# Kernel optimization log

Hardware: AMD Instinct MI355X
Metric: run time of the kernel (lower is better)

The kernel has to match this reference:

```python
import jax, jax.numpy as jnp
import numpy as np

# ---- config constants (from configs) ----
B, L, C = 32, 512, 16
DM, DS, DCONV, EXP, EL = 128, 16, 4, 2, 2
PATCH, STRIDE, PAD, PRED = 16, 8, 8, 96
DIN = EXP * DM            # 256
DTR = (DM + 15) // 16     # dt_rank = 8
NPATCH = (L + 2 * PAD - PATCH) // STRIDE + 1   # 65
HNF = DM * NPATCH         # 8320
EPS = 1e-5


def setup_inputs() -> dict:
    key = jax.random.key(0)
    ks = jax.random.split(key, 14)
    n = jax.random.normal
    A_log = jnp.tile(jnp.log(jnp.arange(1, DS + 1, dtype=jnp.float32)), (EL, DIN, 1))
    return {
        "x_enc": n(ks[0], (B, L, C), jnp.float32),
        "x_mark_enc": n(ks[1], (B, L, 4), jnp.float32),
        "pe_w": n(ks[2], (DM, 1, PATCH), jnp.float32) * (1.0 / np.sqrt(PATCH)),
        "pe_b": n(ks[3], (DM,), jnp.float32) * 0.02,
        "in_proj_w": n(ks[4], (EL, 2 * DIN, DM), jnp.float32) * (1.0 / np.sqrt(DM)),
        "conv_w": n(ks[5], (EL, DIN, DCONV), jnp.float32) * (1.0 / np.sqrt(DCONV)),
        "conv_b": n(ks[6], (EL, DIN), jnp.float32) * 0.02,
        "x_proj_w": n(ks[7], (EL, DTR + 2 * DS, DIN), jnp.float32) * (1.0 / np.sqrt(DIN)),
        "dt_proj_w": n(ks[8], (EL, DIN, DTR), jnp.float32) * (1.0 / np.sqrt(DTR)),
        "dt_proj_b": n(ks[9], (EL, DIN), jnp.float32) * 0.1,
        "A_log": A_log,
        "D": jnp.ones((EL, DIN), jnp.float32),
        "out_proj_w": n(ks[10], (EL, DM, DIN), jnp.float32) * (1.0 / np.sqrt(DIN)),
        "head_w": n(ks[11], (PRED, HNF), jnp.float32) * (1.0 / np.sqrt(HNF)),
    }


def _silu(x):
    return x * jax.nn.sigmoid(x)


def _mamba(x, in_w, cw, cb, xp_w, dtp_w, dtp_b, A_log, Dp, out_w):
    # x: (b, P, DM)
    b = x.shape[0]
    xz = jnp.einsum('bpd,ed->bpe', x, in_w)            # (b, P, 2*DIN)
    xin, z = jnp.split(xz, 2, axis=-1)
    # causal depthwise conv1d over time
    xt = xin.transpose(0, 2, 1)                        # (b, DIN, P)
    conv = jax.lax.conv_general_dilated(
        xt, cw[:, None, :], (1,), [(DCONV - 1, 0)],
        dimension_numbers=('NCH', 'OIH', 'NCH'), feature_group_count=DIN)
    xc = _silu((conv + cb[None, :, None]).transpose(0, 2, 1))   # (b, P, DIN)
    dbc = jnp.einsum('bpd,ed->bpe', xc, xp_w)          # (b, P, DTR+2*DS)
    dt, Bm, Cm = jnp.split(dbc, [DTR, DTR + DS], axis=-1)
    dt = jax.nn.softplus(jnp.einsum('bpr,dr->bpd', dt, dtp_w) + dtp_b)  # (b,P,DIN)
    A = -jnp.exp(A_log)                                # (DIN, DS)

    def step(h, inp):
        dt_t, B_t, C_t, x_t = inp                      # (b,DIN),(b,DS),(b,DS),(b,DIN)
        dA = jnp.exp(dt_t[:, :, None] * A)             # (b,DIN,DS)
        h = dA * h + (dt_t * x_t)[:, :, None] * B_t[:, None, :]
        y = jnp.einsum('bds,bs->bd', h, C_t)
        return h, y

    h0 = jnp.zeros((b, DIN, DS), x.dtype)
    xs = (dt.transpose(1, 0, 2), Bm.transpose(1, 0, 2),
          Cm.transpose(1, 0, 2), xc.transpose(1, 0, 2))
    _, ys = jax.lax.scan(step, h0, xs)                 # (P, b, DIN)
    y = ys.transpose(1, 0, 2) + xc * Dp
    y = y * _silu(z)
    return jnp.einsum('bpd,od->bpo', y, out_w)         # (b, P, DM)


def reference(x_enc, x_mark_enc, pe_w, pe_b, in_proj_w, conv_w, conv_b,
              x_proj_w, dt_proj_w, dt_proj_b, A_log, D, out_proj_w, head_w):
    # RevIN-style normalization (stats detached, as in torch)
    mean = jax.lax.stop_gradient(jnp.mean(x_enc, axis=1, keepdims=True))
    xc = x_enc - mean
    std = jax.lax.stop_gradient(jnp.sqrt(jnp.var(xc, axis=1, keepdims=True) + EPS))
    xn = xc / std                                      # (B, L, C)
    x = xn.transpose(0, 2, 1).reshape(B * C, 1, L)
    # patch embedding conv
    p = jax.lax.conv_general_dilated(
        x, pe_w, (STRIDE,), [(PAD, PAD)],
        dimension_numbers=('NCH', 'OIH', 'NCH')) + pe_b[None, :, None]
    p = p.transpose(0, 2, 1)                           # (B*C, NPATCH, DM)
    for i in range(EL):
        p = _mamba(p, in_proj_w[i], conv_w[i], conv_b[i], x_proj_w[i],
                   dt_proj_w[i], dt_proj_b[i], A_log[i], D[i], out_proj_w[i])
    flat = p.reshape(B * C, HNF)
    head = flat @ head_w.T                             # (B*C, PRED)
    out = head.reshape(B, C, PRED).transpose(0, 2, 1)  # (B, PRED, C)
    return out * std + mean
```

## Files before the change

### kernel.cpp

```cpp
#include <hip/hip_runtime.h>

typedef __attribute__((ext_vector_type(8))) short bf16x8;
typedef __attribute__((ext_vector_type(4))) float f32x4;

#define DEV static __device__ __forceinline__

constexpr int DM   = 128;
constexpr int DIN  = 256;
constexpr int NP   = 65;
constexpr int NSEQ = 512;
constexpr int HNF  = 8320;
constexpr int LOPL = NSEQ*HNF;

constexpr size_t OFF_FLAG = 0;
constexpr size_t OFF_MEAN = 16;
constexpr size_t OFF_STD  = OFF_MEAN + 512;
constexpr size_t OFF_ANEG = OFF_STD  + 512;
constexpr size_t OFF_CONVW= OFF_ANEG + 8192;
constexpr size_t OFF_CONVB= OFF_CONVW+ 2048;
constexpr size_t OFF_DTPB = OFF_CONVB+ 512;
constexpr size_t OFF_DD   = OFF_DTPB + 512;
constexpr size_t OFF_PEWT = OFF_DD   + 512;
constexpr size_t OFF_PEB  = OFF_PEWT + 2048;
constexpr size_t OFF_INF  = OFF_PEB  + 128;
constexpr size_t OFF_XPF  = OFF_INF  + 65536;
constexpr size_t OFF_OPF  = OFF_XPF  + 12288;
constexpr size_t OFF_HDF  = OFF_OPF  + 32768;
constexpr size_t OFF_PA   = OFF_HDF  + 399360;
constexpr size_t OFF_PB   = OFF_PA   + (size_t)NSEQ*HNF;

DEV float b2f(unsigned short u){ union{unsigned v; float f;} x; x.v = ((unsigned)u)<<16; return x.f; }
DEV unsigned short f2b(float f){
  union{float f32; unsigned u;} x; x.f32 = f;
  unsigned r = x.u + 0x7fffu + ((x.u>>16)&1u);
  return (unsigned short)(r>>16);
}
DEV void split2(float v, unsigned short& h, unsigned short& l){
  h = f2b(v); l = f2b(v - b2f(h));
}
DEV float load_in(const void* p, size_t i, int isbf){
  return isbf ? b2f(((const unsigned short*)p)[i]) : ((const float*)p)[i];
}
DEV f32x4 mfma16(bf16x8 a, bf16x8 b, f32x4 c){
  return __builtin_amdgcn_mfma_f32_16x16x32_bf16(a,b,c,0,0,0);
}
constexpr float LOG2E = 1.4426950408889634f;
constexpr float LN2   = 0.6931471805599453f;
DEV float ex2(float x){ float r; asm("v_exp_f32 %0, %1" : "=v"(r) : "v"(x)); return r; }
DEV float lg2(float x){ float r; asm("v_log_f32 %0, %1" : "=v"(r) : "v"(x)); return r; }
DEV float frcp(float x){ float r; asm("v_rcp_f32 %0, %1" : "=v"(r) : "v"(x)); return r; }
DEV float sigm(float x){ return frcp(1.f + ex2(-x*LOG2E)); }
DEV float softplus(float x){
  float t = ex2(-fabsf(x)*LOG2E);
  return fmaxf(x,0.f) + LN2*lg2(1.f + t);
}
DEV int detect_bf16_wave(const void* x, int tid){
  const unsigned short* u = (const unsigned short*)x;
  unsigned short v = u[2*tid];
  int e = (v>>7)&0xff;
  int pred = (v==0) || (e>=100 && e<=141);
  unsigned long long m = __ballot(pred);
  return __popcll(m) >= 48;
}

constexpr int NPREP = 4039;
__global__ void k_pre(const void* x_enc, const void* pe_w, const void* pe_b,
                      const void* in_w, const void* conv_w, const void* conv_b,
                      const void* xp_w, const void* dtp_b,
                      const void* A_log, const void* Dm, const void* op_w,
                      const void* head_w, float* __restrict__ ws)
{
  const int tid = threadIdx.x;
  __shared__ int sflag;
  __shared__ float sx[512];
  __shared__ float spe[16*128];
  __shared__ float spb[128];
  __shared__ float rs[8], rq[8], sm[2];

  if (tid < 64){
    int f = detect_bf16_wave(x_enc, tid);
    if (tid==0) sflag = f;
  }
  __syncthreads();
  const int isbf = sflag;

  if (blockIdx.x < NPREP){
    if (blockIdx.x==0 && tid==0) ws[OFF_FLAG] = (float)isbf;
    size_t i = (size_t)blockIdx.x*256 + tid;
    const size_t nA=8192, nCW=2048, nCB=512, nDB=512, nD=512, nPW=2048, nPB=128;
    const size_t nIN=131072, nXP=24576, nOP=65536, nHD=798720;

    if (i < nA){ ws[OFF_ANEG+i] = -__expf(load_in(A_log,i,isbf)); return; } i -= nA;
    if (i < nCW){ ws[OFF_CONVW+i] = load_in(conv_w,i,isbf); return; } i -= nCW;
    if (i < nCB){ ws[OFF_CONVB+i] = load_in(conv_b,i,isbf); return; } i -= nCB;
    if (i < nDB){ ws[OFF_DTPB+i]  = load_in(dtp_b,i,isbf); return; } i -= nDB;
    if (i < nD){  ws[OFF_DD+i]    = load_in(Dm,i,isbf); return; } i -= nD;
    if (i < nPW){ size_t k=i>>7, dm=i&127; ws[OFF_PEWT+i]=load_in(pe_w, dm*16+k, isbf); return; } i -= nPW;
    if (i < nPB){ ws[OFF_PEB+i]   = load_in(pe_b,i,isbf); return; } i -= nPB;
    if (i < nIN){
      size_t j=i&7, lane=(i>>3)&63, kk=(i>>9)&3, nt=(i>>11)&31, l=i>>16;
      size_t e=nt*16+(lane&15), k=kk*32+((lane>>4)*8)+j;
      ((unsigned short*)(ws+OFF_INF))[i] = f2b(load_in(in_w,(l*512+e)*128+k,isbf)); return;
    } i -= nIN;
    if (i < nXP){
      size_t j=i&7, lane=(i>>3)&63, kk=(i>>9)&7; size_t rest=i>>12;
      size_t nt=rest%3, l=rest/3;
      size_t o=nt*16+(lane&15), k=kk*32+((lane>>4)*8)+j;
      float v = (o<40)? load_in(xp_w,(l*40+o)*256+k,isbf) : 0.f;
      ((unsigned short*)(ws+OFF_XPF))[i] = f2b(v); return;
    } i -= nXP;
    if (i < nOP){
      size_t j=i&7, lane=(i>>3)&63, kk=(i>>9)&7, nt=(i>>12)&7, l=i>>15;
      size_t dm=nt*16+(lane&15), k=kk*32+((lane>>4)*8)+j;
      ((unsigned short*)(ws+OFF_OPF))[i] = f2b(load_in(op_w,(l*128+dm)*256+k,isbf)); return;
    } i -= nOP;
    if (i < nHD){
      size_t j=i&7, lane=(i>>3)&63, t=i>>9;
      size_t kk=t%260, nt=t/260;
      size_t pr=nt*16+(lane&15), k=kk*32+((lane>>4)*8)+j;
      ((unsigned short*)(ws+OFF_HDF))[i] = f2b(load_in(head_w,pr*8320+k,isbf)); return;
    }
    return;
  }

  const int n = blockIdx.x - NPREP;
  const int b = n>>4, c = n&15;

  float v0 = load_in(x_enc, ((size_t)b*512+tid)*16 + c, isbf);
  float v1 = load_in(x_enc, ((size_t)b*512+tid+256)*16 + c, isbf);
  float s = v0+v1, q = v0*v0+v1*v1;
  for (int o=32;o;o>>=1){ s += __shfl_down(s,o,64); q += __shfl_down(q,o,64); }
  const int w = tid>>6, lane = tid&63;
  if (lane==0){ rs[w]=s; rq[w]=q; }
  __syncthreads();
  if (tid==0){
    float S=rs[0]+rs[1]+rs[2]+rs[3], Q=rq[0]+rq[1]+rq[2]+rq[3];
    float mean = S*(1.f/512.f);
    float var = fmaxf(Q*(1.f/512.f)-mean*mean, 0.f);
    float sd = sqrtf(var+1e-5f);
    sm[0]=mean; sm[1]=1.f/sd;
    ws[OFF_MEAN+n]=mean; ws[OFF_STD+n]=sd;
  }
  __syncthreads();
  const float mean=sm[0], rstd=sm[1];
  sx[tid]=(v0-mean)*rstd; sx[tid+256]=(v1-mean)*rstd;
  for (int i=tid;i<2048;i+=256) spe[i]=load_in(pe_w, (size_t)(i&127)*16 + (i>>7), isbf);
  if (tid<128) spb[tid]=load_in(pe_b, tid, isbf);
  __syncthreads();

  unsigned short* pa_hi = (unsigned short*)(ws+OFF_PA);
  unsigned short* pa_lo = pa_hi + LOPL;
  for (int i=tid;i<NP*DM;i+=256){
    int t=i>>7, dm=i&127;
    float acc = spb[dm];
    int j0 = t*8-8;
    #pragma unroll
    for (int k=0;k<16;k++){ int j=j0+k; if ((unsigned)j<512u) acc += sx[j]*spe[k*128+dm]; }
    unsigned short h,lo2; split2(acc,h,lo2);
    pa_hi[(size_t)n*HNF+i] = h;
    pa_lo[(size_t)n*HNF+i] = lo2;
  }
}

__global__ __launch_bounds__(256,2)
void k_layer(int l, const unsigned short* __restrict__ pin,
             unsigned short* __restrict__ pout, float* __restrict__ ws,
             const void* __restrict__ dtp_w_raw)
{
  const int n = blockIdx.x, tid = threadIdx.x;
  const int w = tid>>6, lane = tid&63, ml = lane&15, quad = lane>>4;
  const int isbf = ws[OFF_FLAG] != 0.f;

  __shared__ __align__(16) unsigned char arena[79040];
  unsigned short* s_hi = (unsigned short*)arena;
  unsigned short* s_lo = (unsigned short*)(arena+34320);
  float* s_dbc = (float*)(arena+68640);

  const unsigned short* INF = (const unsigned short*)(ws+OFF_INF) + (size_t)l*65536;
  const unsigned short* XPF = (const unsigned short*)(ws+OFF_XPF) + (size_t)l*12288;
  const unsigned short* OPF = (const unsigned short*)(ws+OFF_OPF) + (size_t)l*32768;
  const unsigned short* phi = pin + (size_t)n*HNF;
  const unsigned short* plo = phi + LOPL;

  for (int pass=0; pass<2; ++pass){
    f32x4 acc[5][2];
    #pragma unroll
    for (int mt=0;mt<5;mt++){
      #pragma unroll
      for (int p2=0;p2<2;p2++){ f32x4 z={0.f,0.f,0.f,0.f}; acc[mt][p2]=z; }
    }
    bf16x8 ah[2][5], al[2][5];
    #pragma unroll
    for (int mt=0;mt<5;mt++){
      int row = mt*16+ml; if (row>64) row=64;
      ah[0][mt] = *(const bf16x8*)&phi[(size_t)row*128 + quad*8];
      al[0][mt] = *(const bf16x8*)&plo[(size_t)row*128 + quad*8];
    }
    #pragma unroll
    for (int kk=0;kk<4;kk++){
      const int cur = kk&1, nxt = cur^1;
      bf16x8 b0 = *(const bf16x8*)&INF[((size_t)((pass*8+w*2+0)*4+kk))*512 + lane*8];
      bf16x8 b1 = *(const bf16x8*)&INF[((size_t)((pass*8+w*2+1)*4+kk))*512 + lane*8];
      if (kk<3){
        #pragma unroll
        for (int mt=0;mt<5;mt++){
          int row = mt*16+ml; if (row>64) row=64;
          ah[nxt][mt] = *(const bf16x8*)&phi[(size_t)row*128 + (kk+1)*32 + quad*8];
          al[nxt][mt] = *(const bf16x8*)&plo[(size_t)row*128 + (kk+1)*32 + quad*8];
        }
      }
      #pragma unroll
      for (int mt=0;mt<5;mt++)
        acc[mt][0] = mfma16(ah[cur][mt],b0,mfma16(al[cur][mt],b0,acc[mt][0]));
      #pragma unroll
      for (int mt=0;mt<5;mt++)
        acc[mt][1] = mfma16(ah[cur][mt],b1,mfma16(al[cur][mt],b1,acc[mt][1]));
    }
    #pragma unroll
    for (int p2=0;p2<2;p2++){
      int e = (pass*8 + w*2 + p2)*16 + ml;
      #pragma unroll
      for (int mt=0;mt<5;mt++){
        #pragma unroll
        for (int r=0;r<4;r++){
          int t = mt*16+quad*4+r;
          if (t<NP){
            unsigned short h,lo2; split2(acc[mt][p2][r],h,lo2);
            s_hi[t*264+e]=h; s_lo[t*264+e]=lo2;
          }
        }
      }
    }
  }
  __syncthreads();

  {
    const int d = tid;
    const float4 wv = ((const float4*)(ws+OFF_CONVW))[l*256+d];
    const float bb = ws[OFF_CONVB + l*256+d];
    float x0=0.f,x1=0.f,x2=0.f;
    int t = 0;
    for (; t+4<=NP; t+=4){
      float xi0 = b2f(s_hi[(t+0)*264+d]) + b2f(s_lo[(t+0)*264+d]);
      float xi1 = b2f(s_hi[(t+1)*264+d]) + b2f(s_lo[(t+1)*264+d]);
      float xi2 = b2f(s_hi[(t+2)*264+d]) + b2f(s_lo[(t+2)*264+d]);
      float xi3 = b2f(s_hi[(t+3)*264+d]) + b2f(s_lo[(t+3)*264+d]);
      float v0 = bb + wv.x*x0  + wv.y*x1  + wv.z*x2  + wv.w*xi0;
      float v1 = bb + wv.x*x1  + wv.y*x2  + wv.z*xi0 + wv.w*xi1;
      float v2 = bb + wv.x*x2  + wv.y*xi0 + wv.z*xi1 + wv.w*xi2;
      float v3 = bb + wv.x*xi0 + wv.y*xi1 + wv.z*xi2 + wv.w*xi3;
      x0=xi1; x1=xi2; x2=xi3;
      float s0 = v0*sigm(v0), s1 = v1*sigm(v1), s2 = v2*sigm(v2), s3 = v3*sigm(v3);
      unsigned short h,lo2;
      split2(s0,h,lo2); s_hi[(t+0)*264+d]=h; s_lo[(t+0)*264+d]=lo2;
      split2(s1,h,lo2); s_hi[(t+1)*264+d]=h; s_lo[(t+1)*264+d]=lo2;
      split2(s2,h,lo2); s_hi[(t+2)*264+d]=h; s_lo[(t+2)*264+d]=lo2;
      split2(s3,h,lo2); s_hi[(t+3)*264+d]=h; s_lo[(t+3)*264+d]=lo2;
    }
    for (; t<NP; ++t){
      float xi = b2f(s_hi[t*264+d]) + b2f(s_lo[t*264+d]);
      float v = bb + wv.x*x0 + wv.y*x1 + wv.z*x2 + wv.w*xi;
      x0=x1; x1=x2; x2=xi;
      float sv = v * sigm(v);
      unsigned short h,lo2; split2(sv,h,lo2);
      s_hi[t*264+d]=h; s_lo[t*264+d]=lo2;
    }
  }
  __syncthreads();

  for (int tile=w; tile<15; tile+=4){
    int mt=tile/3, nt=tile%3;
    f32x4 acc={0.f,0.f,0.f,0.f};
    #pragma unroll
    for (int kk=0;kk<8;kk++){
      int row = mt*16+ml; if (row>64) row=64;
      bf16x8 ah = *(const bf16x8*)&s_hi[row*264 + kk*32 + quad*8];
      bf16x8 al = *(const bf16x8*)&s_lo[row*264 + kk*32 + quad*8];
      bf16x8 b  = *(const bf16x8*)&XPF[((size_t)(nt*8+kk))*512 + lane*8];
      acc = mfma16(ah,b,mfma16(al,b,acc));
    }
    int o = nt*16+ml;
    #pragma unroll
    for (int r=0;r<4;r++){
      int t=mt*16+quad*4+r;
      if (t<NP && o<40) s_dbc[t*40+o] = acc[r];
    }
  }
  __syncthreads();

  {
    const int d = tid;
    float A2[16];
    {
      const float4* ap = (const float4*)(ws+OFF_ANEG) + ((size_t)l*256+d)*4;
      #pragma unroll
      for (int qq=0;qq<4;qq++){
        float4 t4 = ap[qq];
        A2[qq*4]=t4.x*LOG2E; A2[qq*4+1]=t4.y*LOG2E; A2[qq*4+2]=t4.z*LOG2E; A2[qq*4+3]=t4.w*LOG2E;
      }
    }
    int fastbit = 1;
    #pragma unroll
    for (int ss=0;ss<16;ss++){
      float ex = -(float)(ss+1)*LOG2E;
      fastbit &= (fabsf(A2[ss]-ex) <= 1e-4f*(float)(ss+1)) ? 1 : 0;
    }
    const int fastu = __all(fastbit);
    const float Dv = ws[OFF_DD + l*256+d];
    const float bias = ws[OFF_DTPB + l*256+d];
    float wdt[8];
    #pragma unroll
    for (int r=0;r<8;r++) wdt[r] = load_in(dtp_w_raw, ((size_t)l*256+d)*8+r, isbf);
    float h[16];
    #pragma unroll
    for (int ss=0;ss<16;ss++) h[ss]=0.f;

    float4 q0 = *(const float4*)&s_dbc[0];
    float4 q1 = *(const float4*)&s_dbc[4];
    float xh = b2f(s_hi[d]), xl = b2f(s_lo[d]);

    for (int t=0;t<NP;t++){
      const float* row = &s_dbc[t*40];
      float xv = xh + xl;
      float4 b0=*(const float4*)(row+8),  b1=*(const float4*)(row+12),
             b2v=*(const float4*)(row+16), b3=*(const float4*)(row+20);
      float4 c0=*(const float4*)(row+24), c1=*(const float4*)(row+28),
             c2=*(const float4*)(row+32), c3=*(const float4*)(row+36);
      float4 nq0, nq1; float nxh=0.f, nxl=0.f;
      if (t+1<NP){
        const float* nrow = &s_dbc[(t+1)*40];
        nq0 = *(const float4*)(nrow);
        nq1 = *(const float4*)(nrow+4);
        nxh = b2f(s_hi[(t+1)*264+d]); nxl = b2f(s_lo[(t+1)*264+d]);
      }
      float p0 = q0.x*wdt[0] + q0.y*wdt[1];
      float p1 = q0.z*wdt[2] + q0.w*wdt[3];
      float p2 = q1.x*wdt[4] + q1.y*wdt[5];
      float p3 = q1.z*wdt[6] + q1.w*wdt[7];
      float din = (bias + p0 + p1) + (p2 + p3);
      float dtv = softplus(din);
      float dtx = dtv*xv;
      float Bv[16], Cv[16];
      Bv[0]=b0.x;Bv[1]=b0.y;Bv[2]=b0.z;Bv[3]=b0.w; Bv[4]=b1.x;Bv[5]=b1.y;Bv[6]=b1.z;Bv[7]=b1.w;
      Bv[8]=b2v.x;Bv[9]=b2v.y;Bv[10]=b2v.z;Bv[11]=b2v.w; Bv[12]=b3.x;Bv[13]=b3.y;Bv[14]=b3.z;Bv[15]=b3.w;
      Cv[0]=c0.x;Cv[1]=c0.y;Cv[2]=c0.z;Cv[3]=c0.w; Cv[4]=c1.x;Cv[5]=c1.y;Cv[6]=c1.z;Cv[7]=c1.w;
      Cv[8]=c2.x;Cv[9]=c2.y;Cv[10]=c2.z;Cv[11]=c2.w; Cv[12]=c3.x;Cv[13]=c3.y;Cv[14]=c3.z;Cv[15]=c3.w;
      float rr[16];
      if (fastu){
        float r1 = ex2(-dtv*LOG2E);
        float r2=r1*r1;
        float r3=r2*r1, r4=r2*r2;
        float r5=r4*r1, r6=r4*r2, r7=r4*r3, r8=r4*r4;
        rr[0]=r1; rr[1]=r2; rr[2]=r3; rr[3]=r4;
        rr[4]=r5; rr[5]=r6; rr[6]=r7; rr[7]=r8;
        rr[8]=r8*r1; rr[9]=r8*r2; rr[10]=r8*r3; rr[11]=r8*r4;
        rr[12]=r8*r5; rr[13]=r8*r6; rr[14]=r8*r7; rr[15]=r8*r8;
      } else {
        #pragma unroll
        for (int ss=0;ss<16;ss++) rr[ss] = ex2(dtv*A2[ss]);
      }
      float y0 = 0.f, y1 = 0.f;
      #pragma unroll
      for (int ss=0;ss<16;ss+=2){
        h[ss]   = rr[ss]*h[ss]     + dtx*Bv[ss];
        h[ss+1] = rr[ss+1]*h[ss+1] + dtx*Bv[ss+1];
        y0 += h[ss]*Cv[ss];
        y1 += h[ss+1]*Cv[ss+1];
      }
      float g0 = (y0+y1) + xv*Dv;
      unsigned short hh,lo2; split2(g0,hh,lo2);
      s_hi[t*264+d]=hh; s_lo[t*264+d]=lo2;
      q0=nq0; q1=nq1; xh=nxh; xl=nxl;
    }
  }
  __syncthreads();

  {
    bf16x8 ah[2][4], al[2][4];
    {
      int row = ml;
      #pragma unroll
      for (int kk=0;kk<4;kk++){
        ah[0][kk] = *(const bf16x8*)&phi[(size_t)row*128 + kk*32 + quad*8];
        al[0][kk] = *(const bf16x8*)&plo[(size_t)row*128 + kk*32 + quad*8];
      }
    }
    #pragma unroll
    for (int mt=0; mt<5; ++mt){
      const int cur = mt&1, nxt = cur^1;
      if (mt<4){
        int row = (mt+1)*16+ml; if (row>64) row=64;
        #pragma unroll
        for (int kk=0;kk<4;kk++){
          ah[nxt][kk] = *(const bf16x8*)&phi[(size_t)row*128 + kk*32 + quad*8];
          al[nxt][kk] = *(const bf16x8*)&plo[(size_t)row*128 + kk*32 + quad*8];
        }
      }
      #pragma unroll
      for (int j=0;j<4;j++){
        int nt = w + j*4;
        f32x4 acc={0.f,0.f,0.f,0.f};
        #pragma unroll
        for (int kk=0;kk<4;kk++){
          bf16x8 b = *(const bf16x8*)&INF[((size_t)((16+nt)*4+kk))*512 + lane*8];
          acc = mfma16(ah[cur][kk],b,mfma16(al[cur][kk],b,acc));
        }
        int d = nt*16+ml;
        #pragma unroll
        for (int r=0;r<4;r++){
          int t = mt*16+quad*4+r;
          if (t<NP){
            float g0 = b2f(s_hi[t*264+d]) + b2f(s_lo[t*264+d]);
            float zv = acc[r];
            float g = g0 * zv * sigm(zv);
            unsigned short hh,lo2; split2(g,hh,lo2);
            s_hi[t*264+d]=hh; s_lo[t*264+d]=lo2;
          }
        }
      }
    }
  }
  __syncthreads();

  {
    f32x4 acc[5][2];
    #pragma unroll
    for (int mt=0;mt<5;mt++){
      #pragma unroll
      for (int p2=0;p2<2;p2++){ f32x4 z={0.f,0.f,0.f,0.f}; acc[mt][p2]=z; }
    }
    bf16x8 bpre[2][2];
    bpre[0][0] = *(const bf16x8*)&OPF[((size_t)((w*2+0)*8+0))*512 + lane*8];
    bpre[0][1] = *(const bf16x8*)&OPF[((size_t)((w*2+1)*8+0))*512 + lane*8];
    #pragma unroll
    for (int kk=0;kk<8;kk++){
      const int cur = kk&1, nxt = cur^1;
      if (kk<7){
        bpre[nxt][0] = *(const bf16x8*)&OPF[((size_t)((w*2+0)*8+kk+1))*512 + lane*8];
        bpre[nxt][1] = *(const bf16x8*)&OPF[((size_t)((w*2+1)*8+kk+1))*512 + lane*8];
      }
      bf16x8 ah[5], al[5];
      #pragma unroll
      for (int mt=0;mt<5;mt++){
        int row = mt*16+ml; if (row>64) row=64;
        ah[mt] = *(const bf16x8*)&s_hi[row*264 + kk*32 + quad*8];
        al[mt] = *(const bf16x8*)&s_lo[row*264 + kk*32 + quad*8];
      }
      #pragma unroll
      for (int mt=0;mt<5;mt++)
        acc[mt][0] = mfma16(ah[mt],bpre[cur][0],mfma16(al[mt],bpre[cur][0],acc[mt][0]));
      #pragma unroll
      for (int mt=0;mt<5;mt++)
        acc[mt][1] = mfma16(ah[mt],bpre[cur][1],mfma16(al[mt],bpre[cur][1],acc[mt][1]));
    }
    #pragma unroll
    for (int p2=0;p2<2;p2++){
      int dm = (w*2+p2)*16+ml;
      #pragma unroll
      for (int mt=0;mt<5;mt++){
        #pragma unroll
        for (int r=0;r<4;r++){
          int t = mt*16+quad*4+r;
          if (t<NP){
            unsigned short hh,lo2; split2(acc[mt][p2][r],hh,lo2);
            pout[(size_t)n*HNF + t*128 + dm] = hh;
            pout[(size_t)n*HNF + t*128 + dm + LOPL] = lo2;
          }
        }
      }
    }
  }
}

__global__ void k_head(const float* __restrict__ ws, void* __restrict__ out)
{
  const int blk = blockIdx.x;
  const int nt = blk%6, mt = blk/6;
  const int tid = threadIdx.x, w = tid>>6, lane = tid&63, ml = lane&15, quad = lane>>4;
  const unsigned short* pa_hi = (const unsigned short*)(ws+OFF_PA);
  const unsigned short* pa_lo = pa_hi + LOPL;
  const unsigned short* HDF = (const unsigned short*)(ws+OFF_HDF);
  __shared__ float red[4][64][4];

  f32x4 acc={0.f,0.f,0.f,0.f};
  const size_t abase = (size_t)(mt*16+ml)*HNF + quad*8;
  for (int i=0;i<65;i++){
    int kk = w*65+i;
    bf16x8 ah = *(const bf16x8*)(pa_hi + abase + (size_t)kk*32);
    bf16x8 al = *(const bf16x8*)(pa_lo + abase + (size_t)kk*32);
    bf16x8 b = *(const bf16x8*)&HDF[((size_t)(nt*260+kk))*512 + lane*8];
    acc = mfma16(ah,b,mfma16(al,b,acc));
  }
  #pragma unroll
  for (int r=0;r<4;r++) red[w][lane][r]=acc[r];
  __syncthreads();
  if (w==0){
    const int isbf = ws[OFF_FLAG]!=0.f;
    #pragma unroll
    for (int r=0;r<4;r++){
      float s = red[0][lane][r]+red[1][lane][r]+red[2][lane][r]+red[3][lane][r];
      int nseq = mt*16 + quad*4 + r;
      int pred = nt*16 + ml;
      float val = s*ws[OFF_STD+nseq] + ws[OFF_MEAN+nseq];
      size_t o = ((size_t)(nseq>>4)*96 + pred)*16 + (nseq&15);
      if (isbf) ((unsigned short*)out)[o] = f2b(val);
      else      ((float*)out)[o] = val;
    }
  }
}

extern "C" void kernel_launch(void* const* d_in, const int* in_sizes, int n_in,
                              void* d_out, int out_size, void* d_ws, size_t ws_size,
                              hipStream_t stream)
{
  (void)in_sizes; (void)n_in; (void)out_size; (void)ws_size;
  float* ws = (float*)d_ws;
  const void* x_enc = d_in[0];
  const void* pe_w  = d_in[2];  const void* pe_b  = d_in[3];
  const void* in_w  = d_in[4];  const void* conv_w= d_in[5];
  const void* conv_b= d_in[6];  const void* xp_w  = d_in[7];
  const void* dtp_w = d_in[8];  const void* dtp_b = d_in[9];
  const void* A_log = d_in[10]; const void* Dm    = d_in[11];
  const void* op_w  = d_in[12]; const void* head_w= d_in[13];

  k_pre<<<NPREP+NSEQ,256,0,stream>>>(x_enc,pe_w,pe_b,in_w,conv_w,conv_b,xp_w,
                                     dtp_b,A_log,Dm,op_w,head_w,ws);
  unsigned short* pa = (unsigned short*)(ws+OFF_PA);
  unsigned short* pb = (unsigned short*)(ws+OFF_PB);
  k_layer<<<NSEQ,256,0,stream>>>(0,pa,pb,ws,dtp_w);
  k_layer<<<NSEQ,256,0,stream>>>(1,pb,pa,ws,dtp_w);
  k_head<<<192,256,0,stream>>>(ws,d_out);
}
```

Measured before the change: 276.0 us.

## Vectorize weight prep conversion and split head GEMM K across more blocks

The weight-repacking part of the prep kernel now has each thread convert and store 8 bf16 values with vector loads and stores instead of one element per thread, which cuts the prep grid size and index arithmetic. The head GEMM is split along K into 4 partial blocks per output tile (768 blocks instead of 192), writing partial sums into the now-free PB buffer. A new small finalize kernel reduces the partials and applies the denormalization. This adds a kernel launch and a round trip through global memory for the partials in exchange for more parallelism in a head kernel that previously ran few blocks with long serial loops.

```diff
diff --git a/kernel.cpp b/kernel.cpp
--- a/kernel.cpp
+++ b/kernel.cpp
@@ -1,6 +1,7 @@
 #include <hip/hip_runtime.h>
 
 typedef __attribute__((ext_vector_type(8))) short bf16x8;
+typedef __attribute__((ext_vector_type(8))) unsigned short u16x8;
 typedef __attribute__((ext_vector_type(4))) float f32x4;
 
 #define DEV static __device__ __forceinline__
@@ -28,6 +29,7 @@
 constexpr size_t OFF_HDF  = OFF_OPF  + 32768;
 constexpr size_t OFF_PA   = OFF_HDF  + 399360;
 constexpr size_t OFF_PB   = OFF_PA   + (size_t)NSEQ*HNF;
+constexpr size_t OFF_HACC = OFF_PB;
 
 DEV float b2f(unsigned short u){ union{unsigned v; float f;} x; x.v = ((unsigned)u)<<16; return x.f; }
 DEV unsigned short f2b(float f){
@@ -62,8 +64,23 @@
   unsigned long long m = __ballot(pred);
   return __popcll(m) >= 48;
 }
-
-constexpr int NPREP = 4039;
+DEV u16x8 load8_cvt(const void* p, size_t off, int isbf){
+  u16x8 o;
+  if (isbf){
+    o = *(const u16x8*)((const unsigned short*)p + off);
+  } else {
+    const float* s = (const float*)p + off;
+    float4 a = *(const float4*)(s), b = *(const float4*)(s+4);
+    o[0]=f2b(a.x); o[1]=f2b(a.y); o[2]=f2b(a.z); o[3]=f2b(a.w);
+    o[4]=f2b(b.x); o[5]=f2b(b.y); o[6]=f2b(b.z); o[7]=f2b(b.w);
+  }
+  return o;
+}
+
+constexpr size_t N_SMALL = 13952;
+constexpr size_t N_IN8 = 16384, N_XP8 = 3072, N_OP8 = 8192, N_HD8 = 99840;
+constexpr size_t N_BIG8 = N_IN8+N_XP8+N_OP8+N_HD8;
+constexpr int NPREP = (int)((N_SMALL + N_BIG8 + 255)/256);
 __global__ void k_pre(const void* x_enc, const void* pe_w, const void* pe_b,
                       const void* in_w, const void* conv_w, const void* conv_b,
                       const void* xp_w, const void* dtp_b,
@@ -88,39 +105,49 @@
     if (blockIdx.x==0 && tid==0) ws[OFF_FLAG] = (float)isbf;
     size_t i = (size_t)blockIdx.x*256 + tid;
     const size_t nA=8192, nCW=2048, nCB=512, nDB=512, nD=512, nPW=2048, nPB=128;
-    const size_t nIN=131072, nXP=24576, nOP=65536, nHD=798720;
-
-    if (i < nA){ ws[OFF_ANEG+i] = -__expf(load_in(A_log,i,isbf)); return; } i -= nA;
-    if (i < nCW){ ws[OFF_CONVW+i] = load_in(conv_w,i,isbf); return; } i -= nCW;
-    if (i < nCB){ ws[OFF_CONVB+i] = load_in(conv_b,i,isbf); return; } i -= nCB;
-    if (i < nDB){ ws[OFF_DTPB+i]  = load_in(dtp_b,i,isbf); return; } i -= nDB;
-    if (i < nD){  ws[OFF_DD+i]    = load_in(Dm,i,isbf); return; } i -= nD;
-    if (i < nPW){ size_t k=i>>7, dm=i&127; ws[OFF_PEWT+i]=load_in(pe_w, dm*16+k, isbf); return; } i -= nPW;
-    if (i < nPB){ ws[OFF_PEB+i]   = load_in(pe_b,i,isbf); return; } i -= nPB;
-    if (i < nIN){
-      size_t j=i&7, lane=(i>>3)&63, kk=(i>>9)&3, nt=(i>>11)&31, l=i>>16;
-      size_t e=nt*16+(lane&15), k=kk*32+((lane>>4)*8)+j;
-      ((unsigned short*)(ws+OFF_INF))[i] = f2b(load_in(in_w,(l*512+e)*128+k,isbf)); return;
-    } i -= nIN;
-    if (i < nXP){
-      size_t j=i&7, lane=(i>>3)&63, kk=(i>>9)&7; size_t rest=i>>12;
+    if (i < N_SMALL){
+      if (i < nA){ ws[OFF_ANEG+i] = -__expf(load_in(A_log,i,isbf)); return; } i -= nA;
+      if (i < nCW){ ws[OFF_CONVW+i] = load_in(conv_w,i,isbf); return; } i -= nCW;
+      if (i < nCB){ ws[OFF_CONVB+i] = load_in(conv_b,i,isbf); return; } i -= nCB;
+      if (i < nDB){ ws[OFF_DTPB+i]  = load_in(dtp_b,i,isbf); return; } i -= nDB;
+      if (i < nD){  ws[OFF_DD+i]    = load_in(Dm,i,isbf); return; } i -= nD;
+      if (i < nPW){ size_t k=i>>7, dm=i&127; ws[OFF_PEWT+i]=load_in(pe_w, dm*16+k, isbf); return; } i -= nPW;
+      ws[OFF_PEB+i] = load_in(pe_b,i,isbf); return;
+    }
+    size_t i8 = i - N_SMALL;
+    if (i8 >= N_BIG8) return;
+    if (i8 < N_IN8){
+      size_t lane=i8&63, kk=(i8>>6)&3, nt=(i8>>8)&31, l=i8>>13;
+      size_t e=nt*16+(lane&15), k0=kk*32+((lane>>4)*8);
+      ((u16x8*)((unsigned short*)(ws+OFF_INF)))[i8] =
+        load8_cvt(in_w, (l*512+e)*128 + k0, isbf);
+      return;
+    } i8 -= N_IN8;
+    if (i8 < N_XP8){
+      size_t lane=i8&63, kk=(i8>>6)&7; size_t rest=i8>>9;
       size_t nt=rest%3, l=rest/3;
-      size_t o=nt*16+(lane&15), k=kk*32+((lane>>4)*8)+j;
-      float v = (o<40)? load_in(xp_w,(l*40+o)*256+k,isbf) : 0.f;
-      ((unsigned short*)(ws+OFF_XPF))[i] = f2b(v); return;
-    } i -= nXP;
-    if (i < nOP){
-      size_t j=i&7, lane=(i>>3)&63, kk=(i>>9)&7, nt=(i>>12)&7, l=i>>15;
-      size_t dm=nt*16+(lane&15), k=kk*32+((lane>>4)*8)+j;
-      ((unsigned short*)(ws+OFF_OPF))[i] = f2b(load_in(op_w,(l*128+dm)*256+k,isbf)); return;
-    } i -= nOP;
-    if (i < nHD){
-      size_t j=i&7, lane=(i>>3)&63, t=i>>9;
+      size_t o=nt*16+(lane&15), k0=kk*32+((lane>>4)*8);
+      u16x8 v;
+      if (o<40) v = load8_cvt(xp_w, (l*40+o)*256 + k0, isbf);
+      else { u16x8 z = {0,0,0,0,0,0,0,0}; v = z; }
+      ((u16x8*)((unsigned short*)(ws+OFF_XPF)))[i8] = v;
+      return;
+    } i8 -= N_XP8;
+    if (i8 < N_OP8){
+      size_t lane=i8&63, kk=(i8>>6)&7, nt=(i8>>9)&7, l=i8>>12;
+      size_t dm=nt*16+(lane&15), k0=kk*32+((lane>>4)*8);
+      ((u16x8*)((unsigned short*)(ws+OFF_OPF)))[i8] =
+        load8_cvt(op_w, (l*128+dm)*256 + k0, isbf);
+      return;
+    } i8 -= N_OP8;
+    {
+      size_t lane=i8&63, t=i8>>6;
       size_t kk=t%260, nt=t/260;
-      size_t pr=nt*16+(lane&15), k=kk*32+((lane>>4)*8)+j;
-      ((unsigned short*)(ws+OFF_HDF))[i] = f2b(load_in(head_w,pr*8320+k,isbf)); return;
-    }
-    return;
+      size_t pr=nt*16+(lane&15), k0=kk*32+((lane>>4)*8);
+      ((u16x8*)((unsigned short*)(ws+OFF_HDF)))[i8] =
+        load8_cvt(head_w, pr*8320 + k0, isbf);
+      return;
+    }
   }
 
   const int n = blockIdx.x - NPREP;
@@ -472,10 +499,11 @@
   }
 }
 
-__global__ void k_head(const float* __restrict__ ws, void* __restrict__ out)
+__global__ void k_headp(const float* __restrict__ ws, float* __restrict__ hacc)
 {
   const int blk = blockIdx.x;
-  const int nt = blk%6, mt = blk/6;
+  const int p = blk & 3, tile = blk >> 2;
+  const int nt = tile%6, mt = tile/6;
   const int tid = threadIdx.x, w = tid>>6, lane = tid&63, ml = lane&15, quad = lane>>4;
   const unsigned short* pa_hi = (const unsigned short*)(ws+OFF_PA);
   const unsigned short* pa_lo = pa_hi + LOPL;
@@ -484,8 +512,8 @@
 
   f32x4 acc={0.f,0.f,0.f,0.f};
   const size_t abase = (size_t)(mt*16+ml)*HNF + quad*8;
-  for (int i=0;i<65;i++){
-    int kk = w*65+i;
+  for (int i=w; i<65; i+=4){
+    int kk = p*65 + i;
     bf16x8 ah = *(const bf16x8*)(pa_hi + abase + (size_t)kk*32);
     bf16x8 al = *(const bf16x8*)(pa_lo + abase + (size_t)kk*32);
     bf16x8 b = *(const bf16x8*)&HDF[((size_t)(nt*260+kk))*512 + lane*8];
@@ -495,17 +523,31 @@
   for (int r=0;r<4;r++) red[w][lane][r]=acc[r];
   __syncthreads();
   if (w==0){
-    const int isbf = ws[OFF_FLAG]!=0.f;
     #pragma unroll
     for (int r=0;r<4;r++){
       float s = red[0][lane][r]+red[1][lane][r]+red[2][lane][r]+red[3][lane][r];
-      int nseq = mt*16 + quad*4 + r;
-      int pred = nt*16 + ml;
-      float val = s*ws[OFF_STD+nseq] + ws[OFF_MEAN+nseq];
-      size_t o = ((size_t)(nseq>>4)*96 + pred)*16 + (nseq&15);
-      if (isbf) ((unsigned short*)out)[o] = f2b(val);
-      else      ((float*)out)[o] = val;
-    }
+      hacc[((size_t)tile*4 + p)*256 + lane*4 + r] = s;
+    }
+  }
+}
+
+__global__ void k_fin(const float* __restrict__ ws, void* __restrict__ out)
+{
+  const int tile = blockIdx.x;
+  const int nt = tile%6, mt = tile/6;
+  const int lane = threadIdx.x, ml = lane&15, quad = lane>>4;
+  const float* hacc = ws + OFF_HACC;
+  const int isbf = ws[OFF_FLAG]!=0.f;
+  #pragma unroll
+  for (int r=0;r<4;r++){
+    size_t base = (size_t)tile*4*256 + lane*4 + r;
+    float s = hacc[base] + hacc[base+256] + hacc[base+512] + hacc[base+768];
+    int nseq = mt*16 + quad*4 + r;
+    int pred = nt*16 + ml;
+    float val = s*ws[OFF_STD+nseq] + ws[OFF_MEAN+nseq];
+    size_t o = ((size_t)(nseq>>4)*96 + pred)*16 + (nseq&15);
+    if (isbf) ((unsigned short*)out)[o] = f2b(val);
+    else      ((float*)out)[o] = val;
   }
 }
 
@@ -529,5 +571,6 @@
   unsigned short* pb = (unsigned short*)(ws+OFF_PB);
   k_layer<<<NSEQ,256,0,stream>>>(0,pa,pb,ws,dtp_w);
   k_layer<<<NSEQ,256,0,stream>>>(1,pb,pa,ws,dtp_w);
-  k_head<<<192,256,0,stream>>>(ws,d_out);
-}
+  k_headp<<<768,256,0,stream>>>(ws, ws+OFF_HACC);
+  k_fin<<<192,64,0,stream>>>(ws, d_out);
+}
```

Result: faster. 266.0 us, median of 2 (-3.6%).
